# Kernel optimization log

Measured on AMD Instinct MI355X. Metric: run time of the kernel, lower is better.

Reference implementation:

```python
import jax, jax.numpy as jnp
import numpy as np

B, N, E = 2, 2048, 1024   # batch, seq_len, embed_dim (= hidden_dim)
H, HD = 16, 64            # num_heads, head_dim


def setup_inputs() -> dict:
    key = jax.random.key(0)
    ks = jax.random.split(key, 6)
    w = lambda k: jax.random.normal(k, (E, E), jnp.float32) * 0.02
    return {
        "x": jax.random.normal(ks[0], (B, N, E), jnp.float32),
        "Wq": w(ks[1]), "bq": jnp.zeros((E,), jnp.float32),
        "Wk": w(ks[2]), "bk": jnp.zeros((E,), jnp.float32),
        "Wv": w(ks[3]), "bv": jnp.zeros((E,), jnp.float32),
        "Wu": w(ks[4]), "bu": jnp.zeros((E,), jnp.float32),
        "Wo": w(ks[5]), "bo": jnp.zeros((E,), jnp.float32),
        "ln_g": jnp.ones((E,), jnp.float32),
        "ln_b": jnp.zeros((E,), jnp.float32),
    }


def reference(x, Wq, bq, Wk, bk, Wv, bv, Wu, bu, Wo, bo, ln_g, ln_b):
    # projections (torch Linear: x @ W.T + b)
    q = x @ Wq.T + bq
    k = x @ Wk.T + bk
    v = jax.nn.silu(x @ Wv.T + bv)   # uv_act = swish
    u = jax.nn.silu(x @ Wu.T + bu)
    # split heads: [B, N, H*HD] -> [B, H, N, HD]
    split = lambda t: t.reshape(B, N, H, HD).transpose(0, 2, 1, 3)
    q, k, v = split(q), split(k), split(v)
    # non-softmax attention: ReLU on scaled energy (no causal mask)
    energy = jnp.einsum("bhnd,bhmd->bhnm", q, k) / jnp.float32(np.sqrt(HD))
    energy = jax.nn.relu(energy)
    out = jnp.einsum("bhnm,bhmd->bhnd", energy, v)
    # merge heads: [B, H, N, HD] -> [B, N, H*HD]
    out = out.transpose(0, 2, 1, 3).reshape(B, N, H * HD)
    # layernorm over hidden_dim
    mu = out.mean(-1, keepdims=True)
    var = out.var(-1, keepdims=True)
    out = (out - mu) * jax.lax.rsqrt(var + 1e-5) * ln_g + ln_b
    # gate and output projection
    out = u * out
    return out @ Wo.T + bo
```

## Files before the change

### kernel.cpp

```cpp
#include <hip/hip_runtime.h>
#include <stdint.h>

typedef unsigned short u16;
typedef __attribute__((ext_vector_type(8))) short short8;
typedef __attribute__((ext_vector_type(4))) short short4v;
typedef __attribute__((ext_vector_type(4))) float floatx4;
typedef __attribute__((ext_vector_type(4))) int intx4;

#define B_ 2
#define N_ 2048
#define E_ 1024
#define H_ 16
#define HD_ 64
#define M_TOT (B_ * N_)

__device__ __forceinline__ float bf2f(u16 h) {
    union { unsigned u; float f; } c; c.u = ((unsigned)h) << 16; return c.f;
}
__device__ __forceinline__ u16 f2bf(float f) {
    union { float f; unsigned u; } c; c.f = f;
    unsigned r = c.u + 0x7FFFu + ((c.u >> 16) & 1u);
    return (u16)(r >> 16);
}
__device__ __forceinline__ float silu_f(float x) { return x / (1.f + __expf(-x)); }

__device__ __forceinline__ void gll16(const void* g, void* l) {
    __builtin_amdgcn_global_load_lds(
        (const __attribute__((address_space(1))) void*)g,
        (__attribute__((address_space(3))) void*)l,
        16, 0, 0);
}

__device__ __forceinline__ short4v relu_pack(floatx4 s) {
    union { float f; unsigned u; } c0, c1, c2, c3;
    c0.f = fmaxf(s[0], 0.f); c1.f = fmaxf(s[1], 0.f);
    c2.f = fmaxf(s[2], 0.f); c3.f = fmaxf(s[3], 0.f);
    unsigned lo = __builtin_amdgcn_perm(c1.u + 0x8000u, c0.u + 0x8000u, 0x07060302);
    unsigned hi = __builtin_amdgcn_perm(c3.u + 0x8000u, c2.u + 0x8000u, 0x07060302);
    union { unsigned v[2]; short4v s4; } r; r.v[0] = lo; r.v[1] = hi;
    return r.s4;
}

__launch_bounds__(256, 4)
__global__ void cvt6(const float* __restrict__ s0, const float* __restrict__ s1,
                     const float* __restrict__ s2, const float* __restrict__ s3,
                     const float* __restrict__ s4, const float* __restrict__ s5,
                     u16* __restrict__ d0, u16* __restrict__ d1,
                     u16* __restrict__ d2, u16* __restrict__ d3,
                     u16* __restrict__ d4, u16* __restrict__ d5)
{
    const int z = blockIdx.z;
    if (z > 0 && blockIdx.x >= E_ * E_ / 2048) return;
    const float* src = (z == 0) ? s0 : (z == 1) ? s1 : (z == 2) ? s2
                     : (z == 3) ? s3 : (z == 4) ? s4 : s5;
    u16* dst         = (z == 0) ? d0 : (z == 1) ? d1 : (z == 2) ? d2
                     : (z == 3) ? d3 : (z == 4) ? d4 : d5;
    const int i = (blockIdx.x * 256 + threadIdx.x) * 8;
    floatx4 a = *(const floatx4*)(src + i);
    floatx4 b = *(const floatx4*)(src + i + 4);
    union { u16 h[8]; intx4 v; } o;
    o.h[0] = f2bf(a[0]); o.h[1] = f2bf(a[1]); o.h[2] = f2bf(a[2]); o.h[3] = f2bf(a[3]);
    o.h[4] = f2bf(b[0]); o.h[5] = f2bf(b[1]); o.h[6] = f2bf(b[2]); o.h[7] = f2bf(b[3]);
    *(intx4*)(dst + i) = o.v;
}

#define NTILES (E_ / 64)

#define LDA_FRAGS(mlo, BUF)                                                        \
    _Pragma("unroll")                                                              \
    for (int mi = 0; mi < 4; mi++) {                                               \
        af[(mlo) + mi][0] = *(const short8*)&lds[(BUF)*16384 + raA + ((mlo)+mi)*512];        \
        af[(mlo) + mi][1] = *(const short8*)&lds[(BUF)*16384 + raA + 4096 + ((mlo)+mi)*512]; \
    }

#define LDB_FRAGS(blo, BUF)                                                        \
    _Pragma("unroll")                                                              \
    for (int bn = 0; bn < 2; bn++) {                                               \
        bfr[bn][0] = *(const short8*)&lds[32768 + (BUF)*16384 + raB + ((blo)+bn)*512];        \
        bfr[bn][1] = *(const short8*)&lds[32768 + (BUF)*16384 + raB + 4096 + ((blo)+bn)*512]; \
    }

#define MFMAQ(mlo, blo)                                                            \
    _Pragma("unroll")                                                              \
    for (int mi = 0; mi < 4; mi++)                                                 \
        _Pragma("unroll")                                                          \
        for (int bn = 0; bn < 2; bn++) {                                           \
            acc[(mlo)+mi][(blo)+bn] = __builtin_amdgcn_mfma_f32_16x16x32_bf16(     \
                af[(mlo)+mi][0], bfr[bn][0], acc[(mlo)+mi][(blo)+bn], 0, 0, 0);    \
            acc[(mlo)+mi][(blo)+bn] = __builtin_amdgcn_mfma_f32_16x16x32_bf16(     \
                af[(mlo)+mi][1], bfr[bn][1], acc[(mlo)+mi][(blo)+bn], 0, 0, 0);    \
        }

#define STAGE_AH(t2, h, BUFX)                                                      \
    if ((t2) < NTILES) {                                                           \
        gll16(As + (size_t)(h)*128*E_ + (t2)*64,      &lds[(BUFX)*16384 + (h)*8192 + wid*512]);        \
        gll16(As + (size_t)(h)*128*E_ + (t2)*64 + 32, &lds[(BUFX)*16384 + (h)*8192 + 4096 + wid*512]); \
    }

#define STAGE_BH(t1, h, BUFX)                                                      \
    if ((t1) < NTILES) {                                                           \
        gll16(Bs + (size_t)(h)*128*E_ + (t1)*64,      &lds[32768 + (BUFX)*16384 + (h)*8192 + wid*512]);        \
        gll16(Bs + (size_t)(h)*128*E_ + (t1)*64 + 32, &lds[32768 + (BUFX)*16384 + (h)*8192 + 4096 + wid*512]); \
    }

#define TILE(t, BUF) {                                                             \
    LDA_FRAGS(0, BUF); LDB_FRAGS(0, BUF);                                          \
    STAGE_BH((t)+1, 0, (BUF)^1);                                                   \
    __builtin_amdgcn_s_barrier();                                                  \
    __builtin_amdgcn_s_setprio(1); MFMAQ(0, 0); __builtin_amdgcn_s_setprio(0);     \
    __builtin_amdgcn_s_barrier();                                                  \
    LDA_FRAGS(4, BUF);                                                             \
    STAGE_BH((t)+1, 1, (BUF)^1);                                                   \
    __builtin_amdgcn_s_barrier();                                                  \
    __builtin_amdgcn_s_setprio(1); MFMAQ(4, 0); __builtin_amdgcn_s_setprio(0);     \
    __builtin_amdgcn_s_barrier();                                                  \
    LDB_FRAGS(2, BUF);                                                             \
    STAGE_AH((t)+2, 0, BUF);                                                       \
    __builtin_amdgcn_s_barrier();                                                  \
    __builtin_amdgcn_s_setprio(1); MFMAQ(4, 2); __builtin_amdgcn_s_setprio(0);     \
    __builtin_amdgcn_s_barrier();                                                  \
    STAGE_AH((t)+2, 1, BUF);                                                       \
    __builtin_amdgcn_s_barrier();                                                  \
    __builtin_amdgcn_s_setprio(1); MFMAQ(0, 2); __builtin_amdgcn_s_setprio(0);     \
    asm volatile("s_waitcnt vmcnt(4)" ::: "memory");                               \
    __builtin_amdgcn_s_barrier();                                                  \
}

__launch_bounds__(512, 2)
__global__ void gemm8p(const u16* __restrict__ A,
                       const u16* __restrict__ W0, const u16* __restrict__ W1,
                       const u16* __restrict__ W2, const u16* __restrict__ W3,
                       const float* __restrict__ bi0, const float* __restrict__ bi1,
                       const float* __restrict__ bi2, const float* __restrict__ bi3,
                       u16* __restrict__ O0, u16* __restrict__ O1,
                       u16* __restrict__ O2, u16* __restrict__ O3,
                       int actmask, int scalemask)
{
    __shared__ u16 lds[65536];

    const int z = blockIdx.z;
    const u16* Wp   = (z == 0) ? W0 : (z == 1) ? W1 : (z == 2) ? W2 : W3;
    const float* Bi = (z == 0) ? bi0 : (z == 1) ? bi1 : (z == 2) ? bi2 : bi3;
    u16* Out        = (z == 0) ? O0 : (z == 1) ? O1 : (z == 2) ? O2 : O3;
    const bool act = (actmask >> z) & 1;
    const float osc = ((scalemask >> z) & 1) ? 0.125f : 1.0f;

    const int tid = threadIdx.x;
    const int wid = tid >> 6, lane = tid & 63, quad = lane >> 4, l16 = lane & 15;
    const int wm = wid >> 2, wn = wid & 3;
    const int m0 = blockIdx.y * 256;
    const int n0 = blockIdx.x * 256;

    const int swz = ((l16 >> 3) & 1) * 16;
    const int raA = wm * 8192 + l16 * 32 + ((quad * 8) ^ swz);
    const int raB = (wn >> 1) * 8192 + ((wn & 1) * 64 + l16) * 32 + ((quad * 8) ^ swz);

    const int srow_s = tid >> 2;
    const int sce = ((tid & 3) * 8) ^ (((tid >> 5) & 1) * 16);
    const u16* As = A  + (size_t)(m0 + srow_s) * E_ + sce;
    const u16* Bs = Wp + (size_t)(n0 + srow_s) * E_ + sce;

    floatx4 acc[8][4];
    const floatx4 fz = {0.f, 0.f, 0.f, 0.f};
#pragma unroll
    for (int mi = 0; mi < 8; mi++)
#pragma unroll
        for (int bn = 0; bn < 4; bn++) acc[mi][bn] = fz;

    short8 af[8][2], bfr[2][2];

    gll16(As,                  &lds[0     + wid*512]);
    gll16(As + 32,             &lds[4096  + wid*512]);
    gll16(As + 128*E_,         &lds[8192  + wid*512]);
    gll16(As + 128*E_ + 32,    &lds[12288 + wid*512]);
    gll16(Bs,                  &lds[32768 +  0    + wid*512]);
    gll16(Bs + 32,             &lds[32768 + 4096  + wid*512]);
    gll16(Bs + 128*E_,         &lds[32768 + 8192  + wid*512]);
    gll16(Bs + 128*E_ + 32,    &lds[32768 + 12288 + wid*512]);
    gll16(As + 64,             &lds[16384 +  0    + wid*512]);
    gll16(As + 96,             &lds[16384 + 4096  + wid*512]);
    gll16(As + 128*E_ + 64,    &lds[16384 + 8192  + wid*512]);
    gll16(As + 128*E_ + 96,    &lds[16384 + 12288 + wid*512]);
    asm volatile("s_waitcnt vmcnt(4)" ::: "memory");
    __builtin_amdgcn_s_barrier();

    for (int tt = 0; tt < NTILES; tt += 2) {
        TILE(tt, 0);
        TILE(tt + 1, 1);
    }

    float bias_v[4];
#pragma unroll
    for (int bn = 0; bn < 4; bn++) bias_v[bn] = Bi[n0 + wn * 64 + bn * 16 + l16];

#pragma unroll
    for (int mi = 0; mi < 8; mi++) {
        const int row = m0 + wm * 128 + mi * 16 + quad * 4;
#pragma unroll
        for (int bn = 0; bn < 4; bn++) {
            const int col = n0 + wn * 64 + bn * 16 + l16;
#pragma unroll
            for (int r = 0; r < 4; r++) {
                float v = acc[mi][bn][r] + bias_v[bn];
                if (act) v = silu_f(v);
                v *= osc;
                Out[(size_t)(row + r) * E_ + col] = f2bf(v);
            }
        }
    }
}

__launch_bounds__(256, 2)
__global__ void gemm_out(const u16* __restrict__ A, const u16* __restrict__ W,
                         const float* __restrict__ Bi, float* __restrict__ Out,
                         int K)
{
    __shared__ u16 a_lds[3][64 * 32];
    __shared__ u16 b_lds[3][128 * 32];

    const int t    = threadIdx.x;
    const int wave = t >> 6, lane = t & 63, quad = lane >> 4, l16 = lane & 15;
    const int m0 = blockIdx.y * 64;
    const int n0 = blockIdx.x * 128;

    floatx4 acc[4][2];
    const floatx4 fz = {0.f, 0.f, 0.f, 0.f};
    for (int i = 0; i < 4; i++)
        for (int j = 0; j < 2; j++) acc[i][j] = fz;

    const int ar = t >> 2;
    const int ac = (t & 3) * 8;
    const u16* Ag0 = A + (size_t)(m0 + ar) * K + ac;
    const u16* Bg0 = W + (size_t)(n0 + ar) * K + ac;
    const u16* Bg1 = W + (size_t)(n0 + 64 + ar) * K + ac;

    const int nt = K / 32;

#define GO_STAGE(tt, bi) {                                      \
        gll16(Ag0 + (tt) * 32, &a_lds[bi][wave * 512]);         \
        gll16(Bg0 + (tt) * 32, &b_lds[bi][wave * 512]);         \
        gll16(Bg1 + (tt) * 32, &b_lds[bi][2048 + wave * 512]); }

    GO_STAGE(0, 0);
    GO_STAGE(1, 1);
    asm volatile("s_waitcnt vmcnt(3)" ::: "memory");
    __builtin_amdgcn_s_barrier();

    for (int tt = 0; tt < nt; tt++) {
        const int bi = tt % 3;
        if (tt + 2 < nt) {
            const int b2 = (tt + 2) % 3;
            GO_STAGE(tt + 2, b2);
        }
        short8 af[4], bfr[2];
#pragma unroll
        for (int i = 0; i < 4; i++)
            af[i]  = *(const short8*)&a_lds[bi][(i * 16 + l16) * 32 + quad * 8];
#pragma unroll
        for (int j = 0; j < 2; j++)
            bfr[j] = *(const short8*)&b_lds[bi][(wave * 32 + j * 16 + l16) * 32 + quad * 8];
#pragma unroll
        for (int i = 0; i < 4; i++)
#pragma unroll
            for (int j = 0; j < 2; j++)
                acc[i][j] = __builtin_amdgcn_mfma_f32_16x16x32_bf16(af[i], bfr[j], acc[i][j], 0, 0, 0);
        if (tt + 2 < nt) {
            asm volatile("s_waitcnt vmcnt(3)" ::: "memory");
        } else {
            asm volatile("s_waitcnt vmcnt(0)" ::: "memory");
        }
        __builtin_amdgcn_s_barrier();
    }
#undef GO_STAGE

    float bias_v[2];
    for (int j = 0; j < 2; j++) bias_v[j] = Bi[n0 + wave * 32 + j * 16 + l16];

    for (int i = 0; i < 4; i++) {
        const int row = m0 + i * 16 + quad * 4;
        for (int j = 0; j < 2; j++) {
            const int col = n0 + wave * 32 + j * 16 + l16;
            for (int r = 0; r < 4; r++)
                Out[(size_t)(row + r) * E_ + col] = acc[i][j][r] + bias_v[j];
        }
    }
}

#define LK 72
#define LV 72
#define KSPLIT 2
#define KCHUNK (N_ / KSPLIT)
#define NKT (KCHUNK / 64)

__launch_bounds__(256, 2)
__global__ void attn(const u16* __restrict__ Q, const u16* __restrict__ Kk,
                     const u16* __restrict__ V,
                     u16* __restrict__ P0, u16* __restrict__ P1)
{
    __shared__ u16 k_lds[2][64 * LK];
    __shared__ u16 v_lds[2][64 * LV];

    const int bh = blockIdx.y;
    const int b = bh >> 4, h = bh & 15;
    const int z = blockIdx.z;
    u16* __restrict__ Oa = (z == 0) ? P0 : P1;
    const int key_base = z * KCHUNK;

    const int t = threadIdx.x;
    const int wave = t >> 6, lane = t & 63, quad = lane >> 4, l16 = lane & 15;
    const int q0 = blockIdx.x * 256 + wave * 64;
    const size_t base = (size_t)b * N_ * E_ + h * HD_;

    short8 aq[4][2];
    for (int mi = 0; mi < 4; mi++)
        for (int ks = 0; ks < 2; ks++)
            aq[mi][ks] = *(const short8*)(Q + base + (size_t)(q0 + mi * 16 + l16) * E_ + ks * 32 + quad * 8);

    floatx4 o[4][4];
    const floatx4 fz = {0.f, 0.f, 0.f, 0.f};
    for (int mi = 0; mi < 4; mi++)
        for (int nd = 0; nd < 4; nd++) o[mi][nd] = fz;

    const int srow = t >> 2, sseg = (t & 3) * 16;
    const int prow = (srow & 32) + (((srow >> 2) & 1) << 4)
                   + (((srow >> 3) & 3) << 2) + (srow & 3);
    const u16* Ksrc = Kk + base + (size_t)(key_base + srow) * E_ + sseg;
    const u16* Vsrc = V + base + (size_t)(key_base + srow) * E_ + sseg;
    const int kofs = prow * LK + sseg;

    intx4 kv0 = *(const intx4*)(Ksrc);
    intx4 kv1 = *(const intx4*)(Ksrc + 8);
    intx4 vv0 = *(const intx4*)(Vsrc);
    intx4 vv1 = *(const intx4*)(Vsrc + 8);
    {
        *(intx4*)(&k_lds[0][kofs])     = kv0;
        *(intx4*)(&k_lds[0][kofs + 8]) = kv1;
        const u16* v0p = (const u16*)&vv0;
        const u16* v1p = (const u16*)&vv1;
        for (int i = 0; i < 8; i++) {
            v_lds[0][(sseg + i) * LV + srow]     = v0p[i];
            v_lds[0][(sseg + 8 + i) * LV + srow] = v1p[i];
        }
    }

    for (int kt = 0; kt < NKT; kt++) {
        __syncthreads();
        const int cur = kt & 1;

        if (kt + 1 < NKT) {
            const u16* kg = Ksrc + (size_t)((kt + 1) * 64) * E_;
            const u16* vg = Vsrc + (size_t)((kt + 1) * 64) * E_;
            kv0 = *(const intx4*)(kg);
            kv1 = *(const intx4*)(kg + 8);
            vv0 = *(const intx4*)(vg);
            vv1 = *(const intx4*)(vg + 8);
        }

        for (int g = 0; g < 2; g++) {
            short8 ka[2][2];
            for (int tp = 0; tp < 2; tp++)
                for (int ks = 0; ks < 2; ks++)
                    ka[tp][ks] = *(const short8*)&k_lds[cur][(g * 32 + tp * 16 + l16) * LK + ks * 32 + quad * 8];
            short8 bv[4];
            for (int nd = 0; nd < 4; nd++)
                bv[nd] = *(const short8*)&v_lds[cur][(nd * 16 + l16) * LV + g * 32 + quad * 8];

            for (int mi = 0; mi < 4; mi++) {
                floatx4 c0 = __builtin_amdgcn_mfma_f32_16x16x32_bf16(ka[0][0], aq[mi][0], fz, 0, 0, 0);
                c0 = __builtin_amdgcn_mfma_f32_16x16x32_bf16(ka[0][1], aq[mi][1], c0, 0, 0, 0);
                floatx4 c1 = __builtin_amdgcn_mfma_f32_16x16x32_bf16(ka[1][0], aq[mi][0], fz, 0, 0, 0);
                c1 = __builtin_amdgcn_mfma_f32_16x16x32_bf16(ka[1][1], aq[mi][1], c1, 0, 0, 0);
                union { short4v h[2]; short8 s8; } sf;
                sf.h[0] = relu_pack(c0);
                sf.h[1] = relu_pack(c1);
                for (int nd = 0; nd < 4; nd++)
                    o[mi][nd] = __builtin_amdgcn_mfma_f32_16x16x32_bf16(sf.s8, bv[nd], o[mi][nd], 0, 0, 0);
            }
        }

        if (kt + 1 < NKT) {
            const int nxt = cur ^ 1;
            *(intx4*)(&k_lds[nxt][kofs])     = kv0;
            *(intx4*)(&k_lds[nxt][kofs + 8]) = kv1;
            const u16* v0p = (const u16*)&vv0;
            const u16* v1p = (const u16*)&vv1;
            for (int i = 0; i < 8; i++) {
                v_lds[nxt][(sseg + i) * LV + srow]     = v0p[i];
                v_lds[nxt][(sseg + 8 + i) * LV + srow] = v1p[i];
            }
        }
    }

    for (int mi = 0; mi < 4; mi++)
        for (int nd = 0; nd < 4; nd++)
            for (int r = 0; r < 4; r++)
                Oa[(size_t)(b * N_ + q0 + mi * 16 + quad * 4 + r) * E_ + h * HD_ + nd * 16 + l16] =
                    f2bf(o[mi][nd][r]);
}

__launch_bounds__(256, 4)
__global__ void ln_gate(const u16* __restrict__ P0, const u16* __restrict__ P1,
                        const u16* __restrict__ U,
                        const float* __restrict__ G, const float* __restrict__ Bb,
                        u16* __restrict__ Out)
{
    const int row = blockIdx.x;
    const int t = threadIdx.x;
    const size_t idx = (size_t)row * E_ + t * 4;
    const short4v a0 = *(const short4v*)(P0 + idx);
    const short4v a1 = *(const short4v*)(P1 + idx);
    floatx4 v;
    for (int i = 0; i < 4; i++)
        v[i] = bf2f((u16)a0[i]) + bf2f((u16)a1[i]);
    float s  = v[0] + v[1] + v[2] + v[3];
    float ss = v[0] * v[0] + v[1] * v[1] + v[2] * v[2] + v[3] * v[3];
    for (int off = 32; off; off >>= 1) {
        s  += __shfl_down(s, off, 64);
        ss += __shfl_down(ss, off, 64);
    }
    __shared__ float red[8];
    const int wave = t >> 6, lane = t & 63;
    if (lane == 0) { red[wave] = s; red[4 + wave] = ss; }
    __syncthreads();
    const float S  = red[0] + red[1] + red[2] + red[3];
    const float SS = red[4] + red[5] + red[6] + red[7];
    const float mu  = S * (1.f / E_);
    const float var = SS * (1.f / E_) - mu * mu;
    const float rstd = rsqrtf(var + 1e-5f);

    short4v outv;
    for (int i = 0; i < 4; i++) {
        const int e = t * 4 + i;
        float y = (v[i] - mu) * rstd * G[e] + Bb[e];
        y *= bf2f(U[idx + i]);
        outv[i] = (short)f2bf(y);
    }
    *(short4v*)(Out + idx) = outv;
}

extern "C" void kernel_launch(void* const* d_in, const int* in_sizes, int n_in,
                              void* d_out, int out_size, void* d_ws, size_t ws_size,
                              hipStream_t stream)
{
    const float* x   = (const float*)d_in[0];
    const float* Wq  = (const float*)d_in[1];
    const float* bq  = (const float*)d_in[2];
    const float* Wk  = (const float*)d_in[3];
    const float* bk  = (const float*)d_in[4];
    const float* Wv  = (const float*)d_in[5];
    const float* bv  = (const float*)d_in[6];
    const float* Wu  = (const float*)d_in[7];
    const float* bu  = (const float*)d_in[8];
    const float* Wo  = (const float*)d_in[9];
    const float* bo  = (const float*)d_in[10];
    const float* lng = (const float*)d_in[11];
    const float* lnb = (const float*)d_in[12];

    char* ws = (char*)d_ws;
    u16*  qw  = (u16*)(ws);
    u16*  kw  = (u16*)(ws + 8388608);
    u16*  vw  = (u16*)(ws + 16777216);
    u16*  uw  = (u16*)(ws + 25165824);
    u16*  p0  = (u16*)(ws + 33554432);
    u16*  p1  = (u16*)(ws + 41943040);
    u16*  xb  = (u16*)(ws + 50331648);
    u16*  wbq = (u16*)(ws + 58720256);
    u16*  wbk = (u16*)(ws + 60817408);
    u16*  wbv = (u16*)(ws + 62914560);
    u16*  wbu = (u16*)(ws + 65011712);
    u16*  wbo = (u16*)(ws + 67108864);
    u16*  gw  = (u16*)(ws);

    float* out = (float*)d_out;

    cvt6<<<dim3(M_TOT * E_ / 2048, 1, 6), dim3(256, 1, 1), 0, stream>>>(
        x, Wq, Wk, Wv, Wu, Wo, xb, wbq, wbk, wbv, wbu, wbo);
    gemm8p<<<dim3(E_ / 256, M_TOT / 256, 4), dim3(512, 1, 1), 0, stream>>>(
        xb, wbq, wbk, wbv, wbu, bq, bk, bv, bu, qw, kw, vw, uw, 0xC, 0x1);
    attn<<<dim3(N_ / 256, B_ * H_, KSPLIT), dim3(256, 1, 1), 0, stream>>>(qw, kw, vw, p0, p1);
    ln_gate<<<dim3(M_TOT, 1, 1), dim3(256, 1, 1), 0, stream>>>(p0, p1, uw, lng, lnb, gw);
    gemm_out<<<dim3(E_ / 128, M_TOT / 64, 1), dim3(256, 1, 1), 0, stream>>>(gw, wbo, bo, out, E_);
}
```

Baseline: 207.6 us.

## Replace 256x256 ping-pong QKVU GEMM with 128x128 triple-buffered pipeline

Replaces the large 256x256-tile, 8-wave QKVU projection GEMM (manual ping-pong staging with setprio and multiple barriers per tile) with a simpler 128x128-tile, 4-wave kernel. The new kernel streams K in 32-wide steps through a three-stage LDS ring and uses one barrier per step. It launches 1024 blocks instead of 256, which should fill the CUs better and allow 3 blocks per CU. The cost is less operand reuse per block and more global and LDS traffic. It also drops the swizzled LDS layout, which may cause bank conflicts. An unused store_out helper template is added.

```diff
diff --git a/kernel.cpp b/kernel.cpp
--- a/kernel.cpp
+++ b/kernel.cpp
@@ -23,6 +23,10 @@
     return (u16)(r >> 16);
 }
 __device__ __forceinline__ float silu_f(float x) { return x / (1.f + __expf(-x)); }
+
+template <typename T> __device__ __forceinline__ void store_out(T* p, float v);
+template <> __device__ __forceinline__ void store_out<u16>(u16* p, float v)    { *p = f2bf(v); }
+template <> __device__ __forceinline__ void store_out<float>(float* p, float v) { *p = v; }
 
 __device__ __forceinline__ void gll16(const void* g, void* l) {
     __builtin_amdgcn_global_load_lds(
@@ -64,144 +68,98 @@
     *(intx4*)(dst + i) = o.v;
 }
 
-#define NTILES (E_ / 64)
-
-#define LDA_FRAGS(mlo, BUF)                                                        \
-    _Pragma("unroll")                                                              \
-    for (int mi = 0; mi < 4; mi++) {                                               \
-        af[(mlo) + mi][0] = *(const short8*)&lds[(BUF)*16384 + raA + ((mlo)+mi)*512];        \
-        af[(mlo) + mi][1] = *(const short8*)&lds[(BUF)*16384 + raA + 4096 + ((mlo)+mi)*512]; \
-    }
-
-#define LDB_FRAGS(blo, BUF)                                                        \
-    _Pragma("unroll")                                                              \
-    for (int bn = 0; bn < 2; bn++) {                                               \
-        bfr[bn][0] = *(const short8*)&lds[32768 + (BUF)*16384 + raB + ((blo)+bn)*512];        \
-        bfr[bn][1] = *(const short8*)&lds[32768 + (BUF)*16384 + raB + 4096 + ((blo)+bn)*512]; \
-    }
-
-#define MFMAQ(mlo, blo)                                                            \
-    _Pragma("unroll")                                                              \
-    for (int mi = 0; mi < 4; mi++)                                                 \
-        _Pragma("unroll")                                                          \
-        for (int bn = 0; bn < 2; bn++) {                                           \
-            acc[(mlo)+mi][(blo)+bn] = __builtin_amdgcn_mfma_f32_16x16x32_bf16(     \
-                af[(mlo)+mi][0], bfr[bn][0], acc[(mlo)+mi][(blo)+bn], 0, 0, 0);    \
-            acc[(mlo)+mi][(blo)+bn] = __builtin_amdgcn_mfma_f32_16x16x32_bf16(     \
-                af[(mlo)+mi][1], bfr[bn][1], acc[(mlo)+mi][(blo)+bn], 0, 0, 0);    \
-        }
-
-#define STAGE_AH(t2, h, BUFX)                                                      \
-    if ((t2) < NTILES) {                                                           \
-        gll16(As + (size_t)(h)*128*E_ + (t2)*64,      &lds[(BUFX)*16384 + (h)*8192 + wid*512]);        \
-        gll16(As + (size_t)(h)*128*E_ + (t2)*64 + 32, &lds[(BUFX)*16384 + (h)*8192 + 4096 + wid*512]); \
-    }
-
-#define STAGE_BH(t1, h, BUFX)                                                      \
-    if ((t1) < NTILES) {                                                           \
-        gll16(Bs + (size_t)(h)*128*E_ + (t1)*64,      &lds[32768 + (BUFX)*16384 + (h)*8192 + wid*512]);        \
-        gll16(Bs + (size_t)(h)*128*E_ + (t1)*64 + 32, &lds[32768 + (BUFX)*16384 + (h)*8192 + 4096 + wid*512]); \
-    }
-
-#define TILE(t, BUF) {                                                             \
-    LDA_FRAGS(0, BUF); LDB_FRAGS(0, BUF);                                          \
-    STAGE_BH((t)+1, 0, (BUF)^1);                                                   \
-    __builtin_amdgcn_s_barrier();                                                  \
-    __builtin_amdgcn_s_setprio(1); MFMAQ(0, 0); __builtin_amdgcn_s_setprio(0);     \
-    __builtin_amdgcn_s_barrier();                                                  \
-    LDA_FRAGS(4, BUF);                                                             \
-    STAGE_BH((t)+1, 1, (BUF)^1);                                                   \
-    __builtin_amdgcn_s_barrier();                                                  \
-    __builtin_amdgcn_s_setprio(1); MFMAQ(4, 0); __builtin_amdgcn_s_setprio(0);     \
-    __builtin_amdgcn_s_barrier();                                                  \
-    LDB_FRAGS(2, BUF);                                                             \
-    STAGE_AH((t)+2, 0, BUF);                                                       \
-    __builtin_amdgcn_s_barrier();                                                  \
-    __builtin_amdgcn_s_setprio(1); MFMAQ(4, 2); __builtin_amdgcn_s_setprio(0);     \
-    __builtin_amdgcn_s_barrier();                                                  \
-    STAGE_AH((t)+2, 1, BUF);                                                       \
-    __builtin_amdgcn_s_barrier();                                                  \
-    __builtin_amdgcn_s_setprio(1); MFMAQ(0, 2); __builtin_amdgcn_s_setprio(0);     \
-    asm volatile("s_waitcnt vmcnt(4)" ::: "memory");                               \
-    __builtin_amdgcn_s_barrier();                                                  \
-}
-
-__launch_bounds__(512, 2)
-__global__ void gemm8p(const u16* __restrict__ A,
-                       const u16* __restrict__ W0, const u16* __restrict__ W1,
-                       const u16* __restrict__ W2, const u16* __restrict__ W3,
-                       const float* __restrict__ bi0, const float* __restrict__ bi1,
-                       const float* __restrict__ bi2, const float* __restrict__ bi3,
-                       u16* __restrict__ O0, u16* __restrict__ O1,
-                       u16* __restrict__ O2, u16* __restrict__ O3,
-                       int actmask, int scalemask)
-{
-    __shared__ u16 lds[65536];
+__launch_bounds__(256, 3)
+__global__ void gemm_pipe(const u16* __restrict__ A,
+                          const u16* __restrict__ W0, const u16* __restrict__ W1,
+                          const u16* __restrict__ W2, const u16* __restrict__ W3,
+                          const float* __restrict__ bi0, const float* __restrict__ bi1,
+                          const float* __restrict__ bi2, const float* __restrict__ bi3,
+                          u16* __restrict__ O0, u16* __restrict__ O1,
+                          u16* __restrict__ O2, u16* __restrict__ O3,
+                          int actmask, int scalemask, int K)
+{
+    __shared__ u16 a_lds[3][128 * 32];
+    __shared__ u16 b_lds[3][128 * 32];
 
     const int z = blockIdx.z;
-    const u16* Wp   = (z == 0) ? W0 : (z == 1) ? W1 : (z == 2) ? W2 : W3;
+    const u16* W    = (z == 0) ? W0 : (z == 1) ? W1 : (z == 2) ? W2 : W3;
     const float* Bi = (z == 0) ? bi0 : (z == 1) ? bi1 : (z == 2) ? bi2 : bi3;
     u16* Out        = (z == 0) ? O0 : (z == 1) ? O1 : (z == 2) ? O2 : O3;
     const bool act = (actmask >> z) & 1;
     const float osc = ((scalemask >> z) & 1) ? 0.125f : 1.0f;
 
-    const int tid = threadIdx.x;
-    const int wid = tid >> 6, lane = tid & 63, quad = lane >> 4, l16 = lane & 15;
-    const int wm = wid >> 2, wn = wid & 3;
-    const int m0 = blockIdx.y * 256;
-    const int n0 = blockIdx.x * 256;
-
-    const int swz = ((l16 >> 3) & 1) * 16;
-    const int raA = wm * 8192 + l16 * 32 + ((quad * 8) ^ swz);
-    const int raB = (wn >> 1) * 8192 + ((wn & 1) * 64 + l16) * 32 + ((quad * 8) ^ swz);
-
-    const int srow_s = tid >> 2;
-    const int sce = ((tid & 3) * 8) ^ (((tid >> 5) & 1) * 16);
-    const u16* As = A  + (size_t)(m0 + srow_s) * E_ + sce;
-    const u16* Bs = Wp + (size_t)(n0 + srow_s) * E_ + sce;
-
-    floatx4 acc[8][4];
+    const int t    = threadIdx.x;
+    const int wave = t >> 6, lane = t & 63, quad = lane >> 4, l16 = lane & 15;
+    const int wm = wave >> 1, wn = wave & 1;
+    const int m0 = blockIdx.y * 128;
+    const int n0 = blockIdx.x * 128;
+
+    floatx4 acc[4][4];
     const floatx4 fz = {0.f, 0.f, 0.f, 0.f};
 #pragma unroll
-    for (int mi = 0; mi < 8; mi++)
-#pragma unroll
-        for (int bn = 0; bn < 4; bn++) acc[mi][bn] = fz;
-
-    short8 af[8][2], bfr[2][2];
-
-    gll16(As,                  &lds[0     + wid*512]);
-    gll16(As + 32,             &lds[4096  + wid*512]);
-    gll16(As + 128*E_,         &lds[8192  + wid*512]);
-    gll16(As + 128*E_ + 32,    &lds[12288 + wid*512]);
-    gll16(Bs,                  &lds[32768 +  0    + wid*512]);
-    gll16(Bs + 32,             &lds[32768 + 4096  + wid*512]);
-    gll16(Bs + 128*E_,         &lds[32768 + 8192  + wid*512]);
-    gll16(Bs + 128*E_ + 32,    &lds[32768 + 12288 + wid*512]);
-    gll16(As + 64,             &lds[16384 +  0    + wid*512]);
-    gll16(As + 96,             &lds[16384 + 4096  + wid*512]);
-    gll16(As + 128*E_ + 64,    &lds[16384 + 8192  + wid*512]);
-    gll16(As + 128*E_ + 96,    &lds[16384 + 12288 + wid*512]);
+    for (int i = 0; i < 4; i++)
+#pragma unroll
+        for (int j = 0; j < 4; j++) acc[i][j] = fz;
+
+    const int ar = t >> 2;
+    const int ac = (t & 3) * 8;
+    const u16* Ag0 = A + (size_t)(m0 + ar) * K + ac;
+    const u16* Ag1 = A + (size_t)(m0 + 64 + ar) * K + ac;
+    const u16* Bg0 = W + (size_t)(n0 + ar) * K + ac;
+    const u16* Bg1 = W + (size_t)(n0 + 64 + ar) * K + ac;
+
+    const int nt = K / 32;
+
+#define PSTAGE(tt, bi) {                                           \
+        gll16(Ag0 + (tt) * 32, &a_lds[bi][wave * 512]);            \
+        gll16(Ag1 + (tt) * 32, &a_lds[bi][2048 + wave * 512]);     \
+        gll16(Bg0 + (tt) * 32, &b_lds[bi][wave * 512]);            \
+        gll16(Bg1 + (tt) * 32, &b_lds[bi][2048 + wave * 512]); }
+
+    PSTAGE(0, 0);
+    PSTAGE(1, 1);
     asm volatile("s_waitcnt vmcnt(4)" ::: "memory");
     __builtin_amdgcn_s_barrier();
 
-    for (int tt = 0; tt < NTILES; tt += 2) {
-        TILE(tt, 0);
-        TILE(tt + 1, 1);
-    }
+    for (int tt = 0; tt < nt; tt++) {
+        const int bi = tt % 3;
+        if (tt + 2 < nt) {
+            PSTAGE(tt + 2, (tt + 2) % 3);
+        }
+        short8 af[4], bfr[4];
+#pragma unroll
+        for (int i = 0; i < 4; i++)
+            af[i]  = *(const short8*)&a_lds[bi][(wm * 64 + i * 16 + l16) * 32 + quad * 8];
+#pragma unroll
+        for (int j = 0; j < 4; j++)
+            bfr[j] = *(const short8*)&b_lds[bi][(wn * 64 + j * 16 + l16) * 32 + quad * 8];
+#pragma unroll
+        for (int i = 0; i < 4; i++)
+#pragma unroll
+            for (int j = 0; j < 4; j++)
+                acc[i][j] = __builtin_amdgcn_mfma_f32_16x16x32_bf16(af[i], bfr[j], acc[i][j], 0, 0, 0);
+        if (tt + 2 < nt) {
+            asm volatile("s_waitcnt vmcnt(4)" ::: "memory");
+        } else {
+            asm volatile("s_waitcnt vmcnt(0)" ::: "memory");
+        }
+        __builtin_amdgcn_s_barrier();
+    }
+#undef PSTAGE
 
     float bias_v[4];
 #pragma unroll
-    for (int bn = 0; bn < 4; bn++) bias_v[bn] = Bi[n0 + wn * 64 + bn * 16 + l16];
-
-#pragma unroll
-    for (int mi = 0; mi < 8; mi++) {
-        const int row = m0 + wm * 128 + mi * 16 + quad * 4;
-#pragma unroll
-        for (int bn = 0; bn < 4; bn++) {
-            const int col = n0 + wn * 64 + bn * 16 + l16;
+    for (int j = 0; j < 4; j++) bias_v[j] = Bi[n0 + wn * 64 + j * 16 + l16];
+
+#pragma unroll
+    for (int i = 0; i < 4; i++) {
+        const int row = m0 + wm * 64 + i * 16 + quad * 4;
+#pragma unroll
+        for (int j = 0; j < 4; j++) {
+            const int col = n0 + wn * 64 + j * 16 + l16;
 #pragma unroll
             for (int r = 0; r < 4; r++) {
-                float v = acc[mi][bn][r] + bias_v[bn];
+                float v = acc[i][j][r] + bias_v[j];
                 if (act) v = silu_f(v);
                 v *= osc;
                 Out[(size_t)(row + r) * E_ + col] = f2bf(v);
@@ -249,8 +207,7 @@
     for (int tt = 0; tt < nt; tt++) {
         const int bi = tt % 3;
         if (tt + 2 < nt) {
-            const int b2 = (tt + 2) % 3;
-            GO_STAGE(tt + 2, b2);
+            GO_STAGE(tt + 2, (tt + 2) % 3);
         }
         short8 af[4], bfr[2];
 #pragma unroll
@@ -475,8 +432,8 @@
 
     cvt6<<<dim3(M_TOT * E_ / 2048, 1, 6), dim3(256, 1, 1), 0, stream>>>(
         x, Wq, Wk, Wv, Wu, Wo, xb, wbq, wbk, wbv, wbu, wbo);
-    gemm8p<<<dim3(E_ / 256, M_TOT / 256, 4), dim3(512, 1, 1), 0, stream>>>(
-        xb, wbq, wbk, wbv, wbu, bq, bk, bv, bu, qw, kw, vw, uw, 0xC, 0x1);
+    gemm_pipe<<<dim3(8, 32, 4), dim3(256, 1, 1), 0, stream>>>(
+        xb, wbq, wbk, wbv, wbu, bq, bk, bv, bu, qw, kw, vw, uw, 0xC, 0x1, E_);
     attn<<<dim3(N_ / 256, B_ * H_, KSPLIT), dim3(256, 1, 1), 0, stream>>>(qw, kw, vw, p0, p1);
     ln_gate<<<dim3(M_TOT, 1, 1), dim3(256, 1, 1), 0, stream>>>(p0, p1, uw, lng, lnb, gw);
     gemm_out<<<dim3(E_ / 128, M_TOT / 64, 1), dim3(256, 1, 1), 0, stream>>>(gw, wbo, bo, out, E_);
```

After: 226.5 us. 1.09x slower.
